# Kernel optimization log

Hardware: AMD Instinct MI355X
Metric: run time of the kernel (lower is better)

The kernel has to match this reference:

```python
import jax, jax.numpy as jnp
import numpy as np

N_NODES = 100000
FEATS = 128
N_EDGES = 600000


def setup_inputs() -> dict:
    key = jax.random.key(0)
    ks = jax.random.split(key, 8)
    s = 1.0 / np.sqrt(2 * FEATS)
    s2 = 1.0 / np.sqrt(FEATS)
    return {
        "item_feats": jax.random.normal(ks[0], (N_NODES, FEATS), jnp.float32),
        "user_feats": jax.random.normal(ks[1], (N_NODES, FEATS), jnp.float32),
        "W1": jax.random.uniform(ks[2], (FEATS, 2 * FEATS), jnp.float32, -s, s),
        "b1": jax.random.uniform(ks[3], (FEATS,), jnp.float32, -s, s),
        "W2": jax.random.uniform(ks[4], (1, FEATS), jnp.float32, -s2, s2),
        "b2": jax.random.uniform(ks[5], (1,), jnp.float32, -s2, s2),
        "src_idx": jax.random.randint(ks[6], (N_EDGES,), 0, N_NODES, jnp.int64 if jax.config.jax_enable_x64 else jnp.int32),
        "dst_idx": jax.random.randint(ks[7], (N_EDGES,), 0, N_NODES, jnp.int64 if jax.config.jax_enable_x64 else jnp.int32),
    }


def reference(item_feats, user_feats, W1, b1, W2, b2, src_idx, dst_idx):
    # Per-edge gather + concat: h[e] = [item_feats[src[e]], user_feats[dst[e]]]  -> [E, 2F]
    h = jnp.concatenate([item_feats[src_idx], user_feats[dst_idx]], axis=1)
    # fc1 -> ReLU -> fc2 -> squeeze(1)  (torch Linear: y = x @ W.T + b)
    h1 = jax.nn.relu(h @ W1.T + b1)          # [E, F]
    score = (h1 @ W2.T + b2)[:, 0]           # [E]
    return score
```

## Files before the change

kernel.cpp:

```cpp
#include <hip/hip_runtime.h>
#include <hip/hip_bf16.h>

#define NFEATS 128

typedef __attribute__((ext_vector_type(8))) short bf16x8;
typedef __attribute__((ext_vector_type(4))) float f32x4;

__device__ inline short f2bf(float f) {
    union { float f; unsigned u; } c; c.f = f;
    unsigned u = c.u;
    return (short)((u + 0x7FFFu + ((u >> 16) & 1u)) >> 16);
}
__device__ inline float bf2f(short v) {
    union { unsigned u; float f; } c;
    c.u = ((unsigned)(unsigned short)v) << 16;
    return c.f;
}

__global__ __launch_bounds__(256) void precompute_kernel(
    const float* __restrict__ item, const float* __restrict__ user,
    const float* __restrict__ W1, const float* __restrict__ b1,
    short* __restrict__ A, short* __restrict__ B, int n_nodes)
{
    const int which = blockIdx.y;
    const float* __restrict__ X = which ? user : item;
    short* __restrict__ Out = which ? B : A;
    const int k_off = which ? 128 : 0;

    __shared__ short Wlds[128][136];
    const int tid = threadIdx.x;

    for (int idx = tid; idx < 128 * 128; idx += 256) {
        int j = idx >> 7, k = idx & 127;
        Wlds[j][k] = f2bf(W1[j * 256 + k_off + k]);
    }
    __syncthreads();

    const int wave = tid >> 6, lane = tid & 63;
    const int r16 = lane & 15, q = lane >> 4;
    const int row_base = blockIdx.x * 128 + wave * 32;

    bf16x8 afrag[2][4];
#pragma unroll
    for (int m = 0; m < 2; ++m) {
        int row = row_base + m * 16 + r16;
        if (row >= n_nodes) row = n_nodes - 1;
        const float* xr = X + (size_t)row * NFEATS;
#pragma unroll
        for (int kk = 0; kk < 4; ++kk) {
            int k0 = kk * 32 + q * 8;
            float4 lo = *(const float4*)(xr + k0);
            float4 hi = *(const float4*)(xr + k0 + 4);
            bf16x8 f;
            f[0] = f2bf(lo.x); f[1] = f2bf(lo.y); f[2] = f2bf(lo.z); f[3] = f2bf(lo.w);
            f[4] = f2bf(hi.x); f[5] = f2bf(hi.y); f[6] = f2bf(hi.z); f[7] = f2bf(hi.w);
            afrag[m][kk] = f;
        }
    }

    f32x4 acc[2][8];
#pragma unroll
    for (int n = 0; n < 8; ++n) {
        float bv = which ? 0.f : b1[n * 16 + r16];
        f32x4 init = {bv, bv, bv, bv};
        acc[0][n] = init;
        acc[1][n] = init;
    }

#pragma unroll
    for (int n = 0; n < 8; ++n) {
#pragma unroll
        for (int kk = 0; kk < 4; ++kk) {
            bf16x8 wf = *(const bf16x8*)&Wlds[n * 16 + r16][kk * 32 + q * 8];
            acc[0][n] = __builtin_amdgcn_mfma_f32_16x16x32_bf16(afrag[0][kk], wf, acc[0][n], 0, 0, 0);
            acc[1][n] = __builtin_amdgcn_mfma_f32_16x16x32_bf16(afrag[1][kk], wf, acc[1][n], 0, 0, 0);
        }
    }

#pragma unroll
    for (int m = 0; m < 2; ++m) {
#pragma unroll
        for (int r = 0; r < 4; ++r) {
            int row = row_base + m * 16 + q * 4 + r;
            if (row < n_nodes) {
                short* orow = Out + (size_t)row * NFEATS;
#pragma unroll
                for (int n = 0; n < 8; ++n)
                    orow[n * 16 + r16] = f2bf(acc[m][n][r]);
            }
        }
    }
}

__global__ __launch_bounds__(256) void edge_kernel(
    const short* __restrict__ A, const short* __restrict__ B,
    const int* __restrict__ src, const int* __restrict__ dst,
    const float* __restrict__ W2, const float* __restrict__ b2,
    float* __restrict__ out, int n_edges)
{
    const int t = blockIdx.x * 256 + threadIdx.x;
    const int lane16 = threadIdx.x & 15;

    float w2v[8];
#pragma unroll
    for (int j = 0; j < 8; ++j) w2v[j] = W2[lane16 * 8 + j];
    const float b2v = b2[0];

    const int qw = t >> 4;
    const int nqw = (gridDim.x * 256) >> 4;

    for (int e0 = qw; e0 < n_edges; e0 += 2 * nqw) {
        const int e1 = e0 + nqw;
        const bool has1 = e1 < n_edges;

        int s0 = src[e0], d0 = dst[e0];
        int s1 = has1 ? src[e1] : s0;
        int d1 = has1 ? dst[e1] : d0;

        bf16x8 av0 = *(const bf16x8*)(A + (size_t)s0 * NFEATS + lane16 * 8);
        bf16x8 bv0 = *(const bf16x8*)(B + (size_t)d0 * NFEATS + lane16 * 8);
        bf16x8 av1 = *(const bf16x8*)(A + (size_t)s1 * NFEATS + lane16 * 8);
        bf16x8 bv1 = *(const bf16x8*)(B + (size_t)d1 * NFEATS + lane16 * 8);

        float acc0 = 0.f, acc1 = 0.f;
#pragma unroll
        for (int j = 0; j < 8; ++j) {
            float h0 = bf2f(av0[j]) + bf2f(bv0[j]);
            h0 = fmaxf(h0, 0.f);
            acc0 = fmaf(h0, w2v[j], acc0);
            float h1 = bf2f(av1[j]) + bf2f(bv1[j]);
            h1 = fmaxf(h1, 0.f);
            acc1 = fmaf(h1, w2v[j], acc1);
        }
#pragma unroll
        for (int sh = 1; sh <= 8; sh <<= 1) {
            acc0 += __shfl_xor(acc0, sh);
            acc1 += __shfl_xor(acc1, sh);
        }
        if (lane16 == 0) {
            out[e0] = acc0 + b2v;
            if (has1) out[e1] = acc1 + b2v;
        }
    }
}

extern "C" void kernel_launch(void* const* d_in, const int* in_sizes, int n_in,
                              void* d_out, int out_size, void* d_ws, size_t ws_size,
                              hipStream_t stream) {
    const float* item = (const float*)d_in[0];
    const float* user = (const float*)d_in[1];
    const float* W1   = (const float*)d_in[2];
    const float* b1   = (const float*)d_in[3];
    const float* W2   = (const float*)d_in[4];
    const float* b2   = (const float*)d_in[5];
    const int*   src  = (const int*)d_in[6];
    const int*   dst  = (const int*)d_in[7];
    float* out = (float*)d_out;

    const int n_nodes = in_sizes[0] / NFEATS;
    const int n_edges = in_sizes[6];

    short* A = (short*)d_ws;
    short* B = A + (size_t)n_nodes * NFEATS;

    const int nblk = (n_nodes + 127) / 128;
    dim3 grid(nblk, 2);
    precompute_kernel<<<grid, 256, 0, stream>>>(item, user, W1, b1, A, B, n_nodes);

    edge_kernel<<<2048, 256, 0, stream>>>(A, B, src, dst, W2, b2, out, n_edges);
}
```

Measured before the change: 81.71 us.

## Make precompute kernel persistent so each block reuses its LDS weight tile

The precompute kernel now launches half as many blocks per input matrix, and each block loops over two row tiles. The W1 slice is loaded into LDS once per block and reused, which halves the redundant weight loads and bf16 conversions. The W1 load is also vectorised to float4 reads with packed short4 LDS stores. The cost is less parallelism and no overlap between a block's tiles: each block runs its two tiles one after the other with no prefetch.

```diff
diff --git a/kernel.cpp b/kernel.cpp
--- a/kernel.cpp
+++ b/kernel.cpp
@@ -5,6 +5,7 @@
 
 typedef __attribute__((ext_vector_type(8))) short bf16x8;
 typedef __attribute__((ext_vector_type(4))) float f32x4;
+typedef __attribute__((ext_vector_type(4))) short short4v;
 
 __device__ inline short f2bf(float f) {
     union { float f; unsigned u; } c; c.f = f;
@@ -20,73 +21,88 @@
 __global__ __launch_bounds__(256) void precompute_kernel(
     const float* __restrict__ item, const float* __restrict__ user,
     const float* __restrict__ W1, const float* __restrict__ b1,
-    short* __restrict__ A, short* __restrict__ B, int n_nodes)
+    short* __restrict__ A, short* __restrict__ B,
+    int n_nodes, int nblk_half)
 {
-    const int which = blockIdx.y;
+    const int which = (blockIdx.x >= nblk_half) ? 1 : 0;
+    const int tloc  = blockIdx.x - which * nblk_half;
     const float* __restrict__ X = which ? user : item;
     short* __restrict__ Out = which ? B : A;
-    const int k_off = which ? 128 : 0;
+    const int k_off4 = which ? 32 : 0;
 
     __shared__ short Wlds[128][136];
     const int tid = threadIdx.x;
 
-    for (int idx = tid; idx < 128 * 128; idx += 256) {
-        int j = idx >> 7, k = idx & 127;
-        Wlds[j][k] = f2bf(W1[j * 256 + k_off + k]);
+    const float4* W4 = (const float4*)W1;
+    for (int i = tid; i < 128 * 32; i += 256) {
+        int j = i >> 5, c = i & 31;
+        float4 w = W4[j * 64 + k_off4 + c];
+        short4v p;
+        p[0] = f2bf(w.x); p[1] = f2bf(w.y); p[2] = f2bf(w.z); p[3] = f2bf(w.w);
+        *(short4v*)&Wlds[j][c * 4] = p;
     }
-    __syncthreads();
 
     const int wave = tid >> 6, lane = tid & 63;
     const int r16 = lane & 15, q = lane >> 4;
-    const int row_base = blockIdx.x * 128 + wave * 32;
 
-    bf16x8 afrag[2][4];
+    float bv[8];
 #pragma unroll
-    for (int m = 0; m < 2; ++m) {
-        int row = row_base + m * 16 + r16;
-        if (row >= n_nodes) row = n_nodes - 1;
-        const float* xr = X + (size_t)row * NFEATS;
+    for (int n = 0; n < 8; ++n) bv[n] = which ? 0.f : b1[n * 16 + r16];
+
+    __syncthreads();
+
+    const int n_tiles = (n_nodes + 127) >> 7;
+
+    for (int t = tloc; t < n_tiles; t += nblk_half) {
+        const int row_base = t * 128 + wave * 32;
+
+        bf16x8 afrag[2][4];
 #pragma unroll
-        for (int kk = 0; kk < 4; ++kk) {
-            int k0 = kk * 32 + q * 8;
-            float4 lo = *(const float4*)(xr + k0);
-            float4 hi = *(const float4*)(xr + k0 + 4);
-            bf16x8 f;
-            f[0] = f2bf(lo.x); f[1] = f2bf(lo.y); f[2] = f2bf(lo.z); f[3] = f2bf(lo.w);
-            f[4] = f2bf(hi.x); f[5] = f2bf(hi.y); f[6] = f2bf(hi.z); f[7] = f2bf(hi.w);
-            afrag[m][kk] = f;
+        for (int m = 0; m < 2; ++m) {
+            int row = row_base + m * 16 + r16;
+            if (row >= n_nodes) row = n_nodes - 1;
+            const float* xr = X + (size_t)row * NFEATS;
+#pragma unroll
+            for (int kk = 0; kk < 4; ++kk) {
+                int k0 = kk * 32 + q * 8;
+                float4 lo = *(const float4*)(xr + k0);
+                float4 hi = *(const float4*)(xr + k0 + 4);
+                bf16x8 f;
+                f[0] = f2bf(lo.x); f[1] = f2bf(lo.y); f[2] = f2bf(lo.z); f[3] = f2bf(lo.w);
+                f[4] = f2bf(hi.x); f[5] = f2bf(hi.y); f[6] = f2bf(hi.z); f[7] = f2bf(hi.w);
+                afrag[m][kk] = f;
+            }
         }
-    }
 
-    f32x4 acc[2][8];
+        f32x4 acc[2][8];
 #pragma unroll
-    for (int n = 0; n < 8; ++n) {
-        float bv = which ? 0.f : b1[n * 16 + r16];
-        f32x4 init = {bv, bv, bv, bv};
-        acc[0][n] = init;
-        acc[1][n] = init;
-    }
+        for (int n = 0; n < 8; ++n) {
+            f32x4 init = {bv[n], bv[n], bv[n], bv[n]};
+            acc[0][n] = init;
+            acc[1][n] = init;
+        }
 
 #pragma unroll
-    for (int n = 0; n < 8; ++n) {
+        for (int n = 0; n < 8; ++n) {
 #pragma unroll
-        for (int kk = 0; kk < 4; ++kk) {
-            bf16x8 wf = *(const bf16x8*)&Wlds[n * 16 + r16][kk * 32 + q * 8];
-            acc[0][n] = __builtin_amdgcn_mfma_f32_16x16x32_bf16(afrag[0][kk], wf, acc[0][n], 0, 0, 0);
-            acc[1][n] = __builtin_amdgcn_mfma_f32_16x16x32_bf16(afrag[1][kk], wf, acc[1][n], 0, 0, 0);
+            for (int kk = 0; kk < 4; ++kk) {
+                bf16x8 wf = *(const bf16x8*)&Wlds[n * 16 + r16][kk * 32 + q * 8];
+                acc[0][n] = __builtin_amdgcn_mfma_f32_16x16x32_bf16(afrag[0][kk], wf, acc[0][n], 0, 0, 0);
+                acc[1][n] = __builtin_amdgcn_mfma_f32_16x16x32_bf16(afrag[1][kk], wf, acc[1][n], 0, 0, 0);
+            }
         }
-    }
 
 #pragma unroll
-    for (int m = 0; m < 2; ++m) {
+        for (int m = 0; m < 2; ++m) {
 #pragma unroll
-        for (int r = 0; r < 4; ++r) {
-            int row = row_base + m * 16 + q * 4 + r;
-            if (row < n_nodes) {
-                short* orow = Out + (size_t)row * NFEATS;
+            for (int r = 0; r < 4; ++r) {
+                int row = row_base + m * 16 + q * 4 + r;
+                if (row < n_nodes) {
+                    short* orow = Out + (size_t)row * NFEATS;
 #pragma unroll
-                for (int n = 0; n < 8; ++n)
-                    orow[n * 16 + r16] = f2bf(acc[m][n][r]);
+                    for (int n = 0; n < 8; ++n)
+                        orow[n * 16 + r16] = f2bf(acc[m][n][r]);
+                }
             }
         }
     }
@@ -163,9 +179,10 @@
     short* A = (short*)d_ws;
     short* B = A + (size_t)n_nodes * NFEATS;
 
-    const int nblk = (n_nodes + 127) / 128;
-    dim3 grid(nblk, 2);
-    precompute_kernel<<<grid, 256, 0, stream>>>(item, user, W1, b1, A, B, n_nodes);
+    const int n_tiles = (n_nodes + 127) / 128;
+    const int nblk_half = (n_tiles + 1) / 2;
+    precompute_kernel<<<2 * nblk_half, 256, 0, stream>>>(
+        item, user, W1, b1, A, B, n_nodes, nblk_half);
 
     edge_kernel<<<2048, 256, 0, stream>>>(A, B, src, dst, W2, b2, out, n_edges);
 }
```

Measured after the change: 98.54 us. +20.6%, slower.
